# Kernel tuning notes

Hardware: AMD Instinct MI355X
Metric: run time of the kernel (lower is better)

## Reference

```python
import jax, jax.numpy as jnp
import numpy as np

B, D, H, W = 8, 64, 128, 256
NH, NO = 64, 64  # nhidden, noutput


def _lstm_dir(x, Wih, Whh, bih, bhh, reverse=False):
    """Single-direction LSTM over x: [T, B, I] -> [T, B, H]. PyTorch gate order i,f,g,o."""
    if reverse:
        x = x[::-1]
    # Precompute input contribution to gates for all timesteps: [T, B, 4H]
    gx = jnp.einsum('tbi,gi->tbg', x, Wih) + (bih + bhh)
    Hd = Whh.shape[1]

    def step(carry, g):
        h, c = carry
        g = g + h @ Whh.T
        i, f, gg, o = jnp.split(g, 4, axis=-1)
        c = jax.nn.sigmoid(f) * c + jax.nn.sigmoid(i) * jnp.tanh(gg)
        h = jax.nn.sigmoid(o) * jnp.tanh(c)
        return (h, c), h

    Bt = x.shape[1]
    init = (jnp.zeros((Bt, Hd), x.dtype), jnp.zeros((Bt, Hd), x.dtype))
    _, hs = jax.lax.scan(step, init, gx)
    if reverse:
        hs = hs[::-1]
    return hs


def _bilstm(x, pf, pb):
    return jnp.concatenate(
        [_lstm_dir(x, *pf), _lstm_dir(x, *pb, reverse=True)], axis=-1)


def setup_inputs() -> dict:
    key = jax.random.key(0)
    ks = jax.random.split(key, 17)
    bound = 1.0 / np.sqrt(NH)

    def u(k_, shape):
        return jax.random.uniform(k_, shape, jnp.float32, -bound, bound)

    inp = {"img": jax.random.normal(ks[0], (B, D, H, W), jnp.float32)}
    # horizontal LSTM: input D -> hidden NH, bidirectional
    inp["h_Wih_f"] = u(ks[1], (4 * NH, D))
    inp["h_Whh_f"] = u(ks[2], (4 * NH, NH))
    inp["h_bih_f"] = u(ks[3], (4 * NH,))
    inp["h_bhh_f"] = u(ks[4], (4 * NH,))
    inp["h_Wih_b"] = u(ks[5], (4 * NH, D))
    inp["h_Whh_b"] = u(ks[6], (4 * NH, NH))
    inp["h_bih_b"] = u(ks[7], (4 * NH,))
    inp["h_bhh_b"] = u(ks[8], (4 * NH,))
    # vertical LSTM: input 2*NH -> hidden NO, bidirectional
    inp["v_Wih_f"] = u(ks[9], (4 * NO, 2 * NH))
    inp["v_Whh_f"] = u(ks[10], (4 * NO, NO))
    inp["v_bih_f"] = u(ks[11], (4 * NO,))
    inp["v_bhh_f"] = u(ks[12], (4 * NO,))
    inp["v_Wih_b"] = u(ks[13], (4 * NO, 2 * NH))
    inp["v_Whh_b"] = u(ks[14], (4 * NO, NO))
    inp["v_bih_b"] = u(ks[15], (4 * NO,))
    inp["v_bhh_b"] = u(ks[16], (4 * NO,))
    return inp


def reference(img,
              h_Wih_f, h_Whh_f, h_bih_f, h_bhh_f,
              h_Wih_b, h_Whh_b, h_bih_b, h_bhh_b,
              v_Wih_f, v_Whh_f, v_bih_f, v_bhh_f,
              v_Wih_b, v_Whh_b, v_bih_b, v_bhh_b):
    b, d, h, w = img.shape
    # BDHW -> WHBD -> [w, h*b, d]
    hin = jnp.transpose(img, (3, 2, 0, 1)).reshape(w, h * b, d)
    hout = _bilstm(hin,
                   (h_Wih_f, h_Whh_f, h_bih_f, h_bhh_f),
                   (h_Wih_b, h_Whh_b, h_bih_b, h_bhh_b))  # [w, h*b, 2*NH]
    # WHBD -> HWBD -> [h, w*b, 2*NH]
    vin = jnp.transpose(hout.reshape(w, h, b, -1), (1, 0, 2, 3)).reshape(h, w * b, -1)
    vout = _bilstm(vin,
                   (v_Wih_f, v_Whh_f, v_bih_f, v_bhh_f),
                   (v_Wih_b, v_Whh_b, v_bih_b, v_bhh_b))  # [h, w*b, 2*NO]
    # HWBD -> BDHW
    return jnp.transpose(vout.reshape(h, w, b, -1), (2, 3, 0, 1))
```

## Files before the change

### kernel.cpp

```cpp
#include <hip/hip_runtime.h>
#include <cstdint>


typedef _Float16 half8_t __attribute__((ext_vector_type(8)));
typedef float f32x4_t __attribute__((ext_vector_type(4)));

__device__ __forceinline__ float sigm(float x) {
    return __builtin_amdgcn_rcpf(1.0f + __builtin_amdgcn_exp2f(x * -1.44269504f));
}
__device__ __forceinline__ float tanh_(float x) {
    return 1.0f - 2.0f * __builtin_amdgcn_rcpf(1.0f + __builtin_amdgcn_exp2f(x * 2.88539008f));
}

__device__ __forceinline__ void block_sync() {
    asm volatile("s_waitcnt lgkmcnt(0)" ::: "memory");
    __builtin_amdgcn_s_barrier();
    asm volatile("" ::: "memory");
}

__device__ __forceinline__ half8_t load_w8(const float* p) {
    const float4 a = *(const float4*)p;
    const float4 b = *(const float4*)(p + 4);
    half8_t r;
    r[0] = (_Float16)a.x; r[1] = (_Float16)a.y; r[2] = (_Float16)a.z; r[3] = (_Float16)a.w;
    r[4] = (_Float16)b.x; r[5] = (_Float16)b.y; r[6] = (_Float16)b.z; r[7] = (_Float16)b.w;
    return r;
}

__device__ __forceinline__ void flush_chunk(const _Float16* bufCg, _Float16* hout,
                                            int hh0, int b, int dir, int wc0, int t)
{
    const int fm = t >> 5, fwi = (t >> 1) & 15, fhal = t & 1;
    const _Float16* src = bufCg + (fwi * 8 + fm) * 64 + fhal * 32;
    _Float16* dst = hout + ((size_t)(((hh0 + fm) * 8 + b) * 256 + wc0 + fwi) << 7)
                  + dir * 64 + fhal * 32;
    #pragma unroll
    for (int i = 0; i < 4; ++i)
        *(half8_t*)(dst + i * 8) = *(const half8_t*)(src + i * 8);
}

__global__ __launch_bounds__(256) void k_xpose(const float* __restrict__ img, _Float16* __restrict__ xt)
{
    __shared__ float Ts[64 * 65];
    const int t  = threadIdx.x;
    const int wt = blockIdx.x & 3;
    const int hh = (blockIdx.x >> 2) & 127;
    const int b  = blockIdx.x >> 9;
    {
        const int d  = t >> 2;
        const int wq = (t & 3) * 16;
        const float* p = img + (((size_t)(b * 64 + d) * 128 + hh) * 256 + wt * 64 + wq);
        #pragma unroll
        for (int i = 0; i < 4; ++i) {
            const float4 v = *(const float4*)(p + i * 4);
            Ts[d * 65 + wq + i * 4 + 0] = v.x;
            Ts[d * 65 + wq + i * 4 + 1] = v.y;
            Ts[d * 65 + wq + i * 4 + 2] = v.z;
            Ts[d * 65 + wq + i * 4 + 3] = v.w;
        }
    }
    __syncthreads();
    const int wl = t >> 2;
    const int dq = (t & 3) * 16;
    half8_t o0, o1;
    #pragma unroll
    for (int i = 0; i < 8; ++i) o0[i] = (_Float16)Ts[(dq + i) * 65 + wl];
    #pragma unroll
    for (int i = 0; i < 8; ++i) o1[i] = (_Float16)Ts[(dq + 8 + i) * 65 + wl];
    _Float16* dst = xt + ((size_t)((b * 128 + hh) * 256 + wt * 64 + wl) << 6) + dq;
    *(half8_t*)(dst)     = o0;
    *(half8_t*)(dst + 8) = o1;
}

__global__ __launch_bounds__(256) void k_hrec(
    const _Float16* __restrict__ xt,
    const float* __restrict__ wihf, const float* __restrict__ whhf,
    const float* __restrict__ bif,  const float* __restrict__ bhf,
    const float* __restrict__ wihb, const float* __restrict__ whhb,
    const float* __restrict__ bib,  const float* __restrict__ bhb,
    _Float16* __restrict__ hout)
{
    __shared__ __align__(16) _Float16 Hbuf[2 * 1024];
    __shared__ __align__(16) _Float16 bufC[2 * 16 * 8 * 64];
    const int t   = threadIdx.x;
    const int dir = blockIdx.x & 1;
    const int g   = blockIdx.x >> 1;
    const int b   = g & 7;
    const int hh0 = (g >> 3) * 8;
    const int wv  = t >> 6;
    const int l   = t & 63;
    const float* Wih = dir ? wihb : wihf;
    const float* Whh = dir ? whhb : whhf;
    const float* Bi  = dir ? bib  : bif;
    const float* Bh  = dir ? bhb  : bhf;

    half8_t Bf[4][4];
    float bias[4];
    #pragma unroll
    for (int p = 0; p < 4; ++p) {
        const int gate = p * 64 + wv * 16 + (l & 15);
        bias[p] = Bi[gate] + Bh[gate];
        #pragma unroll
        for (int kt = 0; kt < 4; ++kt) {
            const int k0 = kt * 32 + (l >> 4) * 8;
            const float* src = (kt < 2) ? (Wih + gate * 64 + k0) : (Whh + gate * 64 + (k0 - 64));
            Bf[p][kt] = load_w8(src);
        }
    }
    for (int i = t; i < 2048; i += 256) Hbuf[i] = (_Float16)0.0f;

    const int mrow = l & 7;
    const int ko   = l >> 4;
    const _Float16* xb = xt + (((size_t)(b * 128 + hh0 + mrow) * 256) << 6) + ko * 8;

    float c_[4] = {0.f, 0.f, 0.f, 0.f};
    const int col = l & 15;
    const int rq  = l >> 4;
    const int jg  = wv * 16 + col;
    const int hpos = (jg >> 5) * 512 + (((jg >> 3) & 3) * 16) * 8 + (jg & 7);

    const int wA = dir ? 255 : 0;
    const int wB = dir ? 254 : 1;
    half8_t xc0 = *(const half8_t*)(xb + (wA << 6));
    half8_t xc1 = *(const half8_t*)(xb + (wA << 6) + 32);
    half8_t xn0 = *(const half8_t*)(xb + (wB << 6));
    half8_t xn1 = *(const half8_t*)(xb + (wB << 6) + 32);
    f32x4_t accx[4];
    #pragma unroll
    for (int p = 0; p < 4; ++p) {
        f32x4_t a = {bias[p], bias[p], bias[p], bias[p]};
        a = __builtin_amdgcn_mfma_f32_16x16x32_f16(xc0, Bf[p][0], a, 0, 0, 0);
        a = __builtin_amdgcn_mfma_f32_16x16x32_f16(xc1, Bf[p][1], a, 0, 0, 0);
        accx[p] = a;
    }
    __syncthreads();

    for (int s = 0; s < 256; ++s) {
        const int grp = (s >> 4) & 1;
        if ((s & 15) == 0 && s > 0)
            flush_chunk(bufC + (grp ^ 1) * 8192, hout, hh0, b, dir,
                        dir ? (256 - s) : (s - 16), t);

        const int rdo = (s & 1) << 10;
        const half8_t H0 = *(const half8_t*)(Hbuf + rdo + l * 8);
        const half8_t H1 = *(const half8_t*)(Hbuf + rdo + 512 + l * 8);
        f32x4_t acc[4];
        #pragma unroll
        for (int p = 0; p < 4; ++p) {
            f32x4_t a = accx[p];
            a = __builtin_amdgcn_mfma_f32_16x16x32_f16(H0, Bf[p][2], a, 0, 0, 0);
            a = __builtin_amdgcn_mfma_f32_16x16x32_f16(H1, Bf[p][3], a, 0, 0, 0);
            acc[p] = a;
        }
        if (s + 1 < 256) {
            #pragma unroll
            for (int p = 0; p < 4; ++p) {
                f32x4_t a = {bias[p], bias[p], bias[p], bias[p]};
                a = __builtin_amdgcn_mfma_f32_16x16x32_f16(xn0, Bf[p][0], a, 0, 0, 0);
                a = __builtin_amdgcn_mfma_f32_16x16x32_f16(xn1, Bf[p][1], a, 0, 0, 0);
                accx[p] = a;
            }
            if (s + 2 < 256) {
                const int w2 = dir ? (253 - s) : (s + 2);
                xn0 = *(const half8_t*)(xb + (w2 << 6));
                xn1 = *(const half8_t*)(xb + (w2 << 6) + 32);
            }
        }
        float hv[4];
        #pragma unroll
        for (int r = 0; r < 4; ++r) {
            const float gi = acc[0][r];
            const float gf = acc[1][r];
            const float gg = acc[2][r];
            const float go = acc[3][r];
            c_[r] = sigm(gf) * c_[r] + sigm(gi) * tanh_(gg);
            hv[r] = sigm(go) * tanh_(c_[r]);
        }
        const int w   = dir ? (255 - s) : s;
        const int wro = ((s + 1) & 1) << 10;
        if (rq < 2) {
            #pragma unroll
            for (int r = 0; r < 4; ++r) {
                const int m = rq * 4 + r;
                Hbuf[wro + hpos + m * 8] = (_Float16)hv[r];
                bufC[grp * 8192 + ((w & 15) * 8 + m) * 64 + jg] = (_Float16)hv[r];
            }
        }
        block_sync();
    }
    flush_chunk(bufC + 8192, hout, hh0, b, dir, dir ? 0 : 240, t);
}

__global__ __launch_bounds__(256) void k_vrec(
    const _Float16* __restrict__ hout,
    const float* __restrict__ wihf, const float* __restrict__ whhf,
    const float* __restrict__ bif,  const float* __restrict__ bhf,
    const float* __restrict__ wihb, const float* __restrict__ whhb,
    const float* __restrict__ bib,  const float* __restrict__ bhb,
    float* __restrict__ outp)
{
    __shared__ __align__(16) _Float16 Hbuf[2 * 1024];
    const int t   = threadIdx.x;
    const int dir = blockIdx.x & 1;
    const int g   = blockIdx.x >> 1;
    const int b   = g & 7;
    const int w0  = (g >> 3) * 8;
    const int wv  = t >> 6;
    const int l   = t & 63;
    const float* Wih = dir ? wihb : wihf;
    const float* Whh = dir ? whhb : whhf;
    const float* Bi  = dir ? bib  : bif;
    const float* Bh  = dir ? bhb  : bhf;

    half8_t Bf[4][6];
    float bias[4];
    #pragma unroll
    for (int p = 0; p < 4; ++p) {
        const int gate = p * 64 + wv * 16 + (l & 15);
        bias[p] = Bi[gate] + Bh[gate];
        #pragma unroll
        for (int kt = 0; kt < 6; ++kt) {
            const int k0 = kt * 32 + (l >> 4) * 8;
            const float* src = (kt < 4) ? (Wih + gate * 128 + k0) : (Whh + gate * 64 + (k0 - 128));
            Bf[p][kt] = load_w8(src);
        }
    }
    for (int i = t; i < 2048; i += 256) Hbuf[i] = (_Float16)0.0f;

    const int mrow = l & 7;
    const int ko   = l >> 4;
    const _Float16* xb = hout + ((size_t)(b * 256 + w0 + mrow) << 7) + ko * 8;

    float c_[4] = {0.f, 0.f, 0.f, 0.f};
    const int col = l & 15;
    const int rq  = l >> 4;
    const int jg  = wv * 16 + col;
    const int hpos = (jg >> 5) * 512 + (((jg >> 3) & 3) * 16) * 8 + (jg & 7);
    const int ch  = dir * 64 + jg;

    const int hA = dir ? 127 : 0;
    const int hB = dir ? 126 : 1;
    half8_t xc[4], xn[4];
    #pragma unroll
    for (int kt = 0; kt < 4; ++kt) {
        xc[kt] = *(const half8_t*)(xb + ((size_t)hA << 18) + kt * 32);
        xn[kt] = *(const half8_t*)(xb + ((size_t)hB << 18) + kt * 32);
    }
    f32x4_t accx[4];
    #pragma unroll
    for (int p = 0; p < 4; ++p) {
        f32x4_t a = {bias[p], bias[p], bias[p], bias[p]};
        #pragma unroll
        for (int kt = 0; kt < 4; ++kt)
            a = __builtin_amdgcn_mfma_f32_16x16x32_f16(xc[kt], Bf[p][kt], a, 0, 0, 0);
        accx[p] = a;
    }
    __syncthreads();

    for (int s = 0; s < 128; ++s) {
        const int rdo = (s & 1) << 10;
        const half8_t H0 = *(const half8_t*)(Hbuf + rdo + l * 8);
        const half8_t H1 = *(const half8_t*)(Hbuf + rdo + 512 + l * 8);
        f32x4_t acc[4];
        #pragma unroll
        for (int p = 0; p < 4; ++p) {
            f32x4_t a = accx[p];
            a = __builtin_amdgcn_mfma_f32_16x16x32_f16(H0, Bf[p][4], a, 0, 0, 0);
            a = __builtin_amdgcn_mfma_f32_16x16x32_f16(H1, Bf[p][5], a, 0, 0, 0);
            acc[p] = a;
        }
        if (s + 1 < 128) {
            #pragma unroll
            for (int p = 0; p < 4; ++p) {
                f32x4_t a = {bias[p], bias[p], bias[p], bias[p]};
                #pragma unroll
                for (int kt = 0; kt < 4; ++kt)
                    a = __builtin_amdgcn_mfma_f32_16x16x32_f16(xn[kt], Bf[p][kt], a, 0, 0, 0);
                accx[p] = a;
            }
            if (s + 2 < 128) {
                const int h2 = dir ? (125 - s) : (s + 2);
                #pragma unroll
                for (int kt = 0; kt < 4; ++kt)
                    xn[kt] = *(const half8_t*)(xb + ((size_t)h2 << 18) + kt * 32);
            }
        }
        float hv[4];
        #pragma unroll
        for (int r = 0; r < 4; ++r) {
            const float gi = acc[0][r];
            const float gf = acc[1][r];
            const float gg = acc[2][r];
            const float go = acc[3][r];
            c_[r] = sigm(gf) * c_[r] + sigm(gi) * tanh_(gg);
            hv[r] = sigm(go) * tanh_(c_[r]);
        }
        const int hh  = dir ? (127 - s) : s;
        const int wro = ((s + 1) & 1) << 10;
        if (rq < 2) {
            float4 v = make_float4(hv[0], hv[1], hv[2], hv[3]);
            *(float4*)(outp + ((size_t)(b * 128 + ch) * 128 + hh) * 256 + w0 + rq * 4) = v;
            #pragma unroll
            for (int r = 0; r < 4; ++r)
                Hbuf[wro + hpos + (rq * 4 + r) * 8] = (_Float16)hv[r];
        }
        block_sync();
    }
}

extern "C" void kernel_launch(void* const* d_in, const int* in_sizes, int n_in,
                              void* d_out, int out_size, void* d_ws, size_t ws_size,
                              hipStream_t stream)
{
    const float* img   = (const float*)d_in[0];
    const float* hWihF = (const float*)d_in[1];
    const float* hWhhF = (const float*)d_in[2];
    const float* hBiF  = (const float*)d_in[3];
    const float* hBhF  = (const float*)d_in[4];
    const float* hWihB = (const float*)d_in[5];
    const float* hWhhB = (const float*)d_in[6];
    const float* hBiB  = (const float*)d_in[7];
    const float* hBhB  = (const float*)d_in[8];
    const float* vWihF = (const float*)d_in[9];
    const float* vWhhF = (const float*)d_in[10];
    const float* vBiF  = (const float*)d_in[11];
    const float* vBhF  = (const float*)d_in[12];
    const float* vWihB = (const float*)d_in[13];
    const float* vWhhB = (const float*)d_in[14];
    const float* vBiB  = (const float*)d_in[15];
    const float* vBhB  = (const float*)d_in[16];

    _Float16* XT   = (_Float16*)d_ws;
    _Float16* HOUT = (_Float16*)((char*)d_ws + (size_t)33554432);

    k_xpose<<<4096, 256, 0, stream>>>(img, XT);
    k_hrec<<<256, 256, 0, stream>>>(XT, hWihF, hWhhF, hBiF, hBhF,
                                    hWihB, hWhhB, hBiB, hBhB, HOUT);
    k_vrec<<<512, 256, 0, stream>>>(HOUT, vWihF, vWhhF, vBiF, vBhF,
                                    vWihB, vWhhB, vBiB, vBhB, (float*)d_out);

    (void)in_sizes; (void)n_in; (void)out_size; (void)ws_size;
}
```

Measured before the change: 553.4 us.

## Stage vertical LSTM outputs in LDS and flush in chunks; unroll-by-two x prefetch

The vertical recurrence kernel no longer writes scattered float4 stores to global memory on every step. It now buffers 16 timesteps of hidden outputs in a double-buffered 64KB LDS area and flushes each chunk with wider contiguous stores, as the horizontal kernel already does. Both recurrence kernels also unroll the time loop by two, using even/odd register sets so the x prefetch runs three steps ahead without branches. The extra 64KB of LDS per block may reduce occupancy, and the flush work sits inside the serial step loop.

After: 522.1 us. 5.7% less time.

```diff
diff --git a/kernel.cpp b/kernel.cpp
--- a/kernel.cpp
+++ b/kernel.cpp
@@ -37,6 +37,25 @@
     #pragma unroll
     for (int i = 0; i < 4; ++i)
         *(half8_t*)(dst + i * 8) = *(const half8_t*)(src + i * 8);
+}
+
+__device__ __forceinline__ void vflush(const float* Og, float* outp,
+                                       int b, int dir, int w0, int hh0c, int t)
+{
+    const int ch = t & 63;
+    const int hq = t >> 6;
+    #pragma unroll
+    for (int i = 0; i < 4; ++i) {
+        const int hh = hq * 4 + i;
+        float v[8];
+        #pragma unroll
+        for (int w = 0; w < 8; ++w) v[w] = Og[(hh * 8 + w) * 64 + ch];
+        float4 a = make_float4(v[0], v[1], v[2], v[3]);
+        float4 c = make_float4(v[4], v[5], v[6], v[7]);
+        float* dst = outp + ((size_t)(b * 128 + dir * 64 + ch) * 128 + hh0c + hh) * 256 + w0;
+        *(float4*)dst = a;
+        *(float4*)(dst + 4) = c;
+    }
 }
 
 __global__ __launch_bounds__(256) void k_xpose(const float* __restrict__ img, _Float16* __restrict__ xt)
@@ -81,7 +100,7 @@
     _Float16* __restrict__ hout)
 {
     __shared__ __align__(16) _Float16 Hbuf[2 * 1024];
-    __shared__ __align__(16) _Float16 bufC[2 * 16 * 8 * 64];
+    __shared__ __align__(16) _Float16 bufC[2 * 8192];
     const int t   = threadIdx.x;
     const int dir = blockIdx.x & 1;
     const int g   = blockIdx.x >> 1;
@@ -119,23 +138,25 @@
     const int jg  = wv * 16 + col;
     const int hpos = (jg >> 5) * 512 + (((jg >> 3) & 3) * 16) * 8 + (jg & 7);
 
-    const int wA = dir ? 255 : 0;
-    const int wB = dir ? 254 : 1;
-    half8_t xc0 = *(const half8_t*)(xb + (wA << 6));
-    half8_t xc1 = *(const half8_t*)(xb + (wA << 6) + 32);
-    half8_t xn0 = *(const half8_t*)(xb + (wB << 6));
-    half8_t xn1 = *(const half8_t*)(xb + (wB << 6) + 32);
+    auto wof = [&](int s) { int ss = s < 256 ? s : 255; return dir ? (255 - ss) : ss; };
+
+    half8_t xE0 = *(const half8_t*)(xb + (wof(0) << 6));
+    half8_t xE1 = *(const half8_t*)(xb + (wof(0) << 6) + 32);
+    half8_t xO0 = *(const half8_t*)(xb + (wof(1) << 6));
+    half8_t xO1 = *(const half8_t*)(xb + (wof(1) << 6) + 32);
     f32x4_t accx[4];
     #pragma unroll
     for (int p = 0; p < 4; ++p) {
         f32x4_t a = {bias[p], bias[p], bias[p], bias[p]};
-        a = __builtin_amdgcn_mfma_f32_16x16x32_f16(xc0, Bf[p][0], a, 0, 0, 0);
-        a = __builtin_amdgcn_mfma_f32_16x16x32_f16(xc1, Bf[p][1], a, 0, 0, 0);
+        a = __builtin_amdgcn_mfma_f32_16x16x32_f16(xE0, Bf[p][0], a, 0, 0, 0);
+        a = __builtin_amdgcn_mfma_f32_16x16x32_f16(xE1, Bf[p][1], a, 0, 0, 0);
         accx[p] = a;
     }
+    xE0 = *(const half8_t*)(xb + (wof(2) << 6));
+    xE1 = *(const half8_t*)(xb + (wof(2) << 6) + 32);
     __syncthreads();
 
-    for (int s = 0; s < 256; ++s) {
+    auto body = [&](int s, half8_t& xr0, half8_t& xr1) {
         const int grp = (s >> 4) & 1;
         if ((s & 15) == 0 && s > 0)
             flush_chunk(bufC + (grp ^ 1) * 8192, hout, hh0, b, dir,
@@ -152,31 +173,25 @@
             a = __builtin_amdgcn_mfma_f32_16x16x32_f16(H1, Bf[p][3], a, 0, 0, 0);
             acc[p] = a;
         }
-        if (s + 1 < 256) {
-            #pragma unroll
-            for (int p = 0; p < 4; ++p) {
-                f32x4_t a = {bias[p], bias[p], bias[p], bias[p]};
-                a = __builtin_amdgcn_mfma_f32_16x16x32_f16(xn0, Bf[p][0], a, 0, 0, 0);
-                a = __builtin_amdgcn_mfma_f32_16x16x32_f16(xn1, Bf[p][1], a, 0, 0, 0);
-                accx[p] = a;
-            }
-            if (s + 2 < 256) {
-                const int w2 = dir ? (253 - s) : (s + 2);
-                xn0 = *(const half8_t*)(xb + (w2 << 6));
-                xn1 = *(const half8_t*)(xb + (w2 << 6) + 32);
-            }
+        #pragma unroll
+        for (int p = 0; p < 4; ++p) {
+            f32x4_t a = {bias[p], bias[p], bias[p], bias[p]};
+            a = __builtin_amdgcn_mfma_f32_16x16x32_f16(xr0, Bf[p][0], a, 0, 0, 0);
+            a = __builtin_amdgcn_mfma_f32_16x16x32_f16(xr1, Bf[p][1], a, 0, 0, 0);
+            accx[p] = a;
+        }
+        {
+            const int wn = wof(s + 3);
+            xr0 = *(const half8_t*)(xb + (wn << 6));
+            xr1 = *(const half8_t*)(xb + (wn << 6) + 32);
         }
         float hv[4];
         #pragma unroll
         for (int r = 0; r < 4; ++r) {
-            const float gi = acc[0][r];
-            const float gf = acc[1][r];
-            const float gg = acc[2][r];
-            const float go = acc[3][r];
-            c_[r] = sigm(gf) * c_[r] + sigm(gi) * tanh_(gg);
-            hv[r] = sigm(go) * tanh_(c_[r]);
-        }
-        const int w   = dir ? (255 - s) : s;
+            c_[r] = sigm(acc[1][r]) * c_[r] + sigm(acc[0][r]) * tanh_(acc[2][r]);
+            hv[r] = sigm(acc[3][r]) * tanh_(c_[r]);
+        }
+        const int w   = wof(s);
         const int wro = ((s + 1) & 1) << 10;
         if (rq < 2) {
             #pragma unroll
@@ -187,6 +202,11 @@
             }
         }
         block_sync();
+    };
+
+    for (int s2 = 0; s2 < 256; s2 += 2) {
+        body(s2,     xO0, xO1);
+        body(s2 + 1, xE0, xE1);
     }
     flush_chunk(bufC + 8192, hout, hh0, b, dir, dir ? 0 : 240, t);
 }
@@ -200,6 +220,7 @@
     float* __restrict__ outp)
 {
     __shared__ __align__(16) _Float16 Hbuf[2 * 1024];
+    __shared__ __align__(16) float OutS[2 * 16 * 8 * 64];
     const int t   = threadIdx.x;
     const int dir = blockIdx.x & 1;
     const int g   = blockIdx.x >> 1;
@@ -236,15 +257,14 @@
     const int rq  = l >> 4;
     const int jg  = wv * 16 + col;
     const int hpos = (jg >> 5) * 512 + (((jg >> 3) & 3) * 16) * 8 + (jg & 7);
-    const int ch  = dir * 64 + jg;
-
-    const int hA = dir ? 127 : 0;
-    const int hB = dir ? 126 : 1;
-    half8_t xc[4], xn[4];
+
+    auto hof = [&](int s) { int ss = s < 128 ? s : 127; return dir ? (127 - ss) : ss; };
+
+    half8_t xE[4], xO[4];
     #pragma unroll
     for (int kt = 0; kt < 4; ++kt) {
-        xc[kt] = *(const half8_t*)(xb + ((size_t)hA << 18) + kt * 32);
-        xn[kt] = *(const half8_t*)(xb + ((size_t)hB << 18) + kt * 32);
+        xE[kt] = *(const half8_t*)(xb + ((size_t)hof(0) << 18) + kt * 32);
+        xO[kt] = *(const half8_t*)(xb + ((size_t)hof(1) << 18) + kt * 32);
     }
     f32x4_t accx[4];
     #pragma unroll
@@ -252,12 +272,20 @@
         f32x4_t a = {bias[p], bias[p], bias[p], bias[p]};
         #pragma unroll
         for (int kt = 0; kt < 4; ++kt)
-            a = __builtin_amdgcn_mfma_f32_16x16x32_f16(xc[kt], Bf[p][kt], a, 0, 0, 0);
+            a = __builtin_amdgcn_mfma_f32_16x16x32_f16(xE[kt], Bf[p][kt], a, 0, 0, 0);
         accx[p] = a;
     }
+    #pragma unroll
+    for (int kt = 0; kt < 4; ++kt)
+        xE[kt] = *(const half8_t*)(xb + ((size_t)hof(2) << 18) + kt * 32);
     __syncthreads();
 
-    for (int s = 0; s < 128; ++s) {
+    auto body = [&](int s, half8_t (&xr)[4]) {
+        const int grp = (s >> 4) & 1;
+        if ((s & 15) == 0 && s > 0)
+            vflush(OutS + (grp ^ 1) * 8192, outp, b, dir, w0,
+                   dir ? (128 - s) : (s - 16), t);
+
         const int rdo = (s & 1) << 10;
         const half8_t H0 = *(const half8_t*)(Hbuf + rdo + l * 8);
         const half8_t H1 = *(const half8_t*)(Hbuf + rdo + 512 + l * 8);
@@ -269,43 +297,44 @@
             a = __builtin_amdgcn_mfma_f32_16x16x32_f16(H1, Bf[p][5], a, 0, 0, 0);
             acc[p] = a;
         }
-        if (s + 1 < 128) {
+        #pragma unroll
+        for (int p = 0; p < 4; ++p) {
+            f32x4_t a = {bias[p], bias[p], bias[p], bias[p]};
             #pragma unroll
-            for (int p = 0; p < 4; ++p) {
-                f32x4_t a = {bias[p], bias[p], bias[p], bias[p]};
-                #pragma unroll
-                for (int kt = 0; kt < 4; ++kt)
-                    a = __builtin_amdgcn_mfma_f32_16x16x32_f16(xn[kt], Bf[p][kt], a, 0, 0, 0);
-                accx[p] = a;
-            }
-            if (s + 2 < 128) {
-                const int h2 = dir ? (125 - s) : (s + 2);
-                #pragma unroll
-                for (int kt = 0; kt < 4; ++kt)
-                    xn[kt] = *(const half8_t*)(xb + ((size_t)h2 << 18) + kt * 32);
-            }
+            for (int kt = 0; kt < 4; ++kt)
+                a = __builtin_amdgcn_mfma_f32_16x16x32_f16(xr[kt], Bf[p][kt], a, 0, 0, 0);
+            accx[p] = a;
+        }
+        {
+            const int hn = hof(s + 3);
+            #pragma unroll
+            for (int kt = 0; kt < 4; ++kt)
+                xr[kt] = *(const half8_t*)(xb + ((size_t)hn << 18) + kt * 32);
         }
         float hv[4];
         #pragma unroll
         for (int r = 0; r < 4; ++r) {
-            const float gi = acc[0][r];
-            const float gf = acc[1][r];
-            const float gg = acc[2][r];
-            const float go = acc[3][r];
-            c_[r] = sigm(gf) * c_[r] + sigm(gi) * tanh_(gg);
-            hv[r] = sigm(go) * tanh_(c_[r]);
-        }
-        const int hh  = dir ? (127 - s) : s;
+            c_[r] = sigm(acc[1][r]) * c_[r] + sigm(acc[0][r]) * tanh_(acc[2][r]);
+            hv[r] = sigm(acc[3][r]) * tanh_(c_[r]);
+        }
+        const int hh  = hof(s);
         const int wro = ((s + 1) & 1) << 10;
         if (rq < 2) {
-            float4 v = make_float4(hv[0], hv[1], hv[2], hv[3]);
-            *(float4*)(outp + ((size_t)(b * 128 + ch) * 128 + hh) * 256 + w0 + rq * 4) = v;
             #pragma unroll
-            for (int r = 0; r < 4; ++r)
-                Hbuf[wro + hpos + (rq * 4 + r) * 8] = (_Float16)hv[r];
+            for (int r = 0; r < 4; ++r) {
+                const int m = rq * 4 + r;
+                Hbuf[wro + hpos + m * 8] = (_Float16)hv[r];
+                OutS[grp * 8192 + ((hh & 15) * 8 + m) * 64 + jg] = hv[r];
+            }
         }
         block_sync();
-    }
+    };
+
+    for (int s2 = 0; s2 < 128; s2 += 2) {
+        body(s2,     xO);
+        body(s2 + 1, xE);
+    }
+    vflush(OutS + 8192, outp, b, dir, w0, dir ? 0 : 112, t);
 }
 
 extern "C" void kernel_launch(void* const* d_in, const int* in_sizes, int n_in,
```
